# Kernel optimization log

Measured on AMD Instinct MI355X. Metric: run time of the kernel, lower is better.

## Reference

```python
import jax, jax.numpy as jnp
import numpy as np

# cfg constants (PatchNet / LDIF defaults)
SOFT_TRANSFER_SCALE = 100.0
LEVEL_SET = -0.07
INTERIOR_POINT_WEIGHT = 10.0
USE_CONSTANTS = True
AGGREGATE_COVERAGE_WITH_MAX = False

B, N, K = 8, 32768, 64


def setup_inputs() -> dict:
    key = jax.random.key(0)
    k1, k2, k3, k4, k5 = jax.random.split(key, 5)
    points_with_sdf = jax.random.normal(k1, (B, N, 4), dtype=jnp.float32)
    # negative constants = interior blobs (SIF convention)
    constants = -jnp.abs(jax.random.normal(k2, (B, K), dtype=jnp.float32))
    # positive anisotropic radii, bounded away from zero
    scales = jax.random.uniform(k3, (B, K, 3), dtype=jnp.float32) + 0.1
    rotations = jax.random.normal(k4, (B, K, 3), dtype=jnp.float32)
    centers = jax.random.normal(k5, (B, K, 3), dtype=jnp.float32)
    return {
        "points_with_sdf": points_with_sdf,
        "constants": constants,
        "scales": scales,
        "rotations": rotations,
        "centers": centers,
        "epoch": 1,
    }


def roll_pitch_yaw_to_rotation_matrices(rpy):
    # rpy: [B, K, 3] -> [B, K, 3, 3]
    c = jnp.cos(rpy)
    s = jnp.sin(rpy)
    cx, cy, cz = c[..., 0], c[..., 1], c[..., 2]
    sx, sy, sz = s[..., 0], s[..., 1], s[..., 2]
    r = jnp.stack([
        cz * cy, cz * sy * sx - sz * cx, cz * sy * cx + sz * sx,
        sz * cy, sz * sy * sx + cz * cx, sz * sy * cx - cz * sx,
        -sy, cy * sx, cy * cx,
    ], axis=-1)
    return r.reshape(rpy.shape[:-1] + (3, 3))


def sample_rbf_surface(points, constants, scales, rotations, centers,
                       use_constants, aggregate_with_max):
    # points: [B,N,3]; per-element params: [B,K,...]
    rot = roll_pitch_yaw_to_rotation_matrices(rotations)          # [B,K,3,3]
    diff = points[:, :, None, :] - centers[:, None, :, :]        # [B,N,K,3]
    # world -> local frame: R^T @ diff
    local = jnp.einsum('bkji,bnkj->bnki', rot, diff)             # [B,N,K,3]
    dist2 = jnp.sum((local / scales[:, None, :, :]) ** 2, axis=-1)  # [B,N,K]
    weights = jnp.exp(-0.5 * dist2)                              # [B,N,K]
    if use_constants:
        weights = constants[:, None, :] * weights
    if aggregate_with_max:
        return jnp.min(weights, axis=-1)  # most negative = strongest coverage
    return jnp.sum(weights, axis=-1)                             # [B,N]


def compute_inverse_occupancy(vals, soft_transfer_scale, level_set):
    return jax.nn.sigmoid(soft_transfer_scale * (vals - level_set))


def reference(points_with_sdf, constants, scales, rotations, centers, epoch):
    points = points_with_sdf[:, :, :3]
    is_outside = points_with_sdf[:, :, 3] > 0
    class_gt = is_outside.astype(jnp.float32)
    sdf_pred = sample_rbf_surface(points, constants, scales, rotations,
                                  centers, USE_CONSTANTS,
                                  AGGREGATE_COVERAGE_WITH_MAX)
    class_pred = compute_inverse_occupancy(sdf_pred, SOFT_TRANSFER_SCALE,
                                           LEVEL_SET)
    # (visualization branch of the original skipped: epoch % vis_epoch != 0)
    weights = class_gt + INTERIOR_POINT_WEIGHT * (1.0 - class_gt)
    diff = class_gt - class_pred
    loss = jnp.mean(weights * diff * diff)
    return loss
```

## Files before the change

### kernel.cpp

```cpp
#include <hip/hip_runtime.h>
#include <math.h>

#define KCL 64
#define NPTS 32768
#define NBATCH 8
#define BLOCK 256
#define PPT 4
#define PTS_PER_BLOCK (BLOCK * PPT)
#define NBLOCKS (NBATCH * NPTS / PTS_PER_BLOCK)
#define BLOCKS_PER_B (NPTS / PTS_PER_BLOCK)

__global__ __launch_bounds__(BLOCK) void point_loss_kernel(
    const float4* __restrict__ pts,
    const float*  __restrict__ constants,
    const float*  __restrict__ scales,
    const float*  __restrict__ rotations,
    const float*  __restrict__ centers,
    float*        __restrict__ partials)
{
    __shared__ float4 cl4[KCL][3];
    __shared__ float wave_sums[BLOCK / 64];

    const int tid = threadIdx.x;
    const int b   = blockIdx.x / BLOCKS_PER_B;

    if (tid < KCL) {
        const int base = b * KCL + tid;
        const float rx = rotations[3 * base + 0];
        const float ry = rotations[3 * base + 1];
        const float rz = rotations[3 * base + 2];
        const float sx = sinf(rx), cx = cosf(rx);
        const float sy = sinf(ry), cy = cosf(ry);
        const float sz = sinf(rz), cz = cosf(rz);

        float R[3][3];
        R[0][0] = cz * cy; R[0][1] = cz * sy * sx - sz * cx; R[0][2] = cz * sy * cx + sz * sx;
        R[1][0] = sz * cy; R[1][1] = sz * sy * sx + cz * cx; R[1][2] = sz * sy * cx - cz * sx;
        R[2][0] = -sy;     R[2][1] = cy * sx;                R[2][2] = cy * cx;

        const float SC = 0.84932184f;
        const float inv[3] = { SC / scales[3 * base + 0],
                               SC / scales[3 * base + 1],
                               SC / scales[3 * base + 2] };
        const float c0 = centers[3 * base + 0];
        const float c1 = centers[3 * base + 1];
        const float c2 = centers[3 * base + 2];

        float M[3][3], q[3];
        #pragma unroll
        for (int i = 0; i < 3; ++i) {
            M[i][0] = R[0][i] * inv[i];
            M[i][1] = R[1][i] * inv[i];
            M[i][2] = R[2][i] * inv[i];
            q[i] = M[i][0] * c0 + M[i][1] * c1 + M[i][2] * c2;
        }
        float A[3][3], t[3];
        #pragma unroll
        for (int j = 0; j < 3; ++j) {
            #pragma unroll
            for (int l = 0; l < 3; ++l)
                A[j][l] = M[0][j] * M[0][l] + M[1][j] * M[1][l] + M[2][j] * M[2][l];
            t[j] = M[0][j] * q[0] + M[1][j] * q[1] + M[2][j] * q[2];
        }
        const float cst = constants[base];
        const float G9 = -(q[0]*q[0] + q[1]*q[1] + q[2]*q[2]) + log2f(-cst);

        cl4[tid][0] = make_float4(-A[0][0], -A[1][1], -A[2][2], -2.0f * A[0][1]);
        cl4[tid][1] = make_float4(-2.0f * A[0][2], -2.0f * A[1][2], 2.0f * t[0], 2.0f * t[1]);
        cl4[tid][2] = make_float4(2.0f * t[2], G9, 0.0f, 0.0f);
    }
    __syncthreads();

    const int n0 = b * NPTS + (blockIdx.x % BLOCKS_PER_B) * PTS_PER_BLOCK + tid;
    float4 p[PPT];
    #pragma unroll
    for (int j = 0; j < PPT; ++j) p[j] = pts[n0 + j * BLOCK];

    float X[PPT], Y[PPT], Z[PPT], X2[PPT], Y2[PPT], Z2[PPT], XY[PPT], XZ[PPT], YZ[PPT];
    #pragma unroll
    for (int j = 0; j < PPT; ++j) {
        X[j] = p[j].x; Y[j] = p[j].y; Z[j] = p[j].z;
        X2[j] = X[j] * X[j]; Y2[j] = Y[j] * Y[j]; Z2[j] = Z[j] * Z[j];
        XY[j] = X[j] * Y[j]; XZ[j] = X[j] * Z[j]; YZ[j] = Y[j] * Z[j];
    }

    float acc[PPT] = {0.0f, 0.0f, 0.0f, 0.0f};
    #pragma unroll 4
    for (int k = 0; k < KCL; ++k) {
        const float4 A  = cl4[k][0];
        const float4 Bv = cl4[k][1];
        const float4 C  = cl4[k][2];
        #pragma unroll
        for (int j = 0; j < PPT; ++j) {
            float s = fmaf(A.x, X2[j],
                      fmaf(A.y, Y2[j],
                      fmaf(A.z, Z2[j],
                      fmaf(A.w, XY[j],
                      fmaf(Bv.x, XZ[j],
                      fmaf(Bv.y, YZ[j],
                      fmaf(Bv.z, X[j],
                      fmaf(Bv.w, Y[j],
                      fmaf(C.x, Z[j], C.y)))))))));
            acc[j] += __builtin_amdgcn_exp2f(s);
        }
    }

    float term = 0.0f;
    #pragma unroll
    for (int j = 0; j < PPT; ++j) {
        const float sdf = -acc[j];
        const float gt  = (p[j].w > 0.0f) ? 1.0f : 0.0f;
        const float z   = 100.0f * (sdf + 0.07f);
        const float pr  = 1.0f / (1.0f + __builtin_amdgcn_exp2f(-1.44269504f * z));
        const float w   = 10.0f - 9.0f * gt;
        const float d   = gt - pr;
        term = fmaf(w * d, d, term);
    }

    #pragma unroll
    for (int off = 32; off > 0; off >>= 1)
        term += __shfl_down(term, off, 64);

    if ((tid & 63) == 0) wave_sums[tid >> 6] = term;
    __syncthreads();

    if (tid == 0) {
        float s = 0.0f;
        #pragma unroll
        for (int i = 0; i < BLOCK / 64; ++i) s += wave_sums[i];
        partials[blockIdx.x] = s;
    }
}

__global__ __launch_bounds__(256) void reduce_kernel(
    const float* __restrict__ partials,
    float*       __restrict__ out)
{
    __shared__ float wave_sums[4];
    const int tid = threadIdx.x;
    float s = partials[tid];

    #pragma unroll
    for (int off = 32; off > 0; off >>= 1)
        s += __shfl_down(s, off, 64);

    if ((tid & 63) == 0) wave_sums[tid >> 6] = s;
    __syncthreads();

    if (tid == 0) {
        float t = wave_sums[0] + wave_sums[1] + wave_sums[2] + wave_sums[3];
        out[0] = t * (1.0f / (NBATCH * (float)NPTS));
    }
}

extern "C" void kernel_launch(void* const* d_in, const int* in_sizes, int n_in,
                              void* d_out, int out_size, void* d_ws, size_t ws_size,
                              hipStream_t stream) {
    const float4* pts       = (const float4*)d_in[0];
    const float*  constants = (const float*)d_in[1];
    const float*  scales    = (const float*)d_in[2];
    const float*  rotations = (const float*)d_in[3];
    const float*  centers   = (const float*)d_in[4];
    float* out      = (float*)d_out;
    float* partials = (float*)d_ws;

    point_loss_kernel<<<NBLOCKS, BLOCK, 0, stream>>>(
        pts, constants, scales, rotations, centers, partials);
    reduce_kernel<<<1, 256, 0, stream>>>(partials, out);
}
```

Baseline: 16.20 us.

## Fuse final reduction into main kernel via flag spin-wait and Horner quadratic form

Removes the separate reduce kernel launch. Block 0 spins on per-block release/acquire flags, sums all partials itself and resets the flags for the next call. The inner loop now evaluates the quadratic form in Horner style on raw x,y,z instead of keeping precomputed products, which frees registers. It also prefetches the next cluster's coefficients from shared memory. The spin-wait relies on every other block being able to run while block 0 waits, which holds here with 256 blocks, and on the workspace flags starting at zero, which only matters for correctness if the magic value is already present.

Result: slower. 19.04 us (+17.6%).

```diff
diff --git a/kernel.cpp b/kernel.cpp
--- a/kernel.cpp
+++ b/kernel.cpp
@@ -9,6 +9,8 @@
 #define PTS_PER_BLOCK (BLOCK * PPT)
 #define NBLOCKS (NBATCH * NPTS / PTS_PER_BLOCK)
 #define BLOCKS_PER_B (NPTS / PTS_PER_BLOCK)
+#define MAGIC 0x5F3C0DE5u
+
 
 __global__ __launch_bounds__(BLOCK) void point_loss_kernel(
     const float4* __restrict__ pts,
@@ -16,13 +18,16 @@
     const float*  __restrict__ scales,
     const float*  __restrict__ rotations,
     const float*  __restrict__ centers,
-    float*        __restrict__ partials)
+    float*        __restrict__ partials,
+    unsigned int* __restrict__ flags,
+    float*        __restrict__ out)
 {
     __shared__ float4 cl4[KCL][3];
     __shared__ float wave_sums[BLOCK / 64];
 
     const int tid = threadIdx.x;
-    const int b   = blockIdx.x / BLOCKS_PER_B;
+    const int bid = blockIdx.x;
+    const int b   = bid / BLOCKS_PER_B;
 
     if (tid < KCL) {
         const int base = b * KCL + tid;
@@ -63,53 +68,46 @@
             t[j] = M[0][j] * q[0] + M[1][j] * q[1] + M[2][j] * q[2];
         }
         const float cst = constants[base];
-        const float G9 = -(q[0]*q[0] + q[1]*q[1] + q[2]*q[2]) + log2f(-cst);
+        const float g9 = log2f(-cst) - (q[0]*q[0] + q[1]*q[1] + q[2]*q[2]);
 
-        cl4[tid][0] = make_float4(-A[0][0], -A[1][1], -A[2][2], -2.0f * A[0][1]);
-        cl4[tid][1] = make_float4(-2.0f * A[0][2], -2.0f * A[1][2], 2.0f * t[0], 2.0f * t[1]);
-        cl4[tid][2] = make_float4(2.0f * t[2], G9, 0.0f, 0.0f);
+        cl4[tid][0] = make_float4(-A[0][0], -2.0f * A[0][1], -2.0f * A[0][2], 2.0f * t[0]);
+        cl4[tid][1] = make_float4(-A[1][1], -2.0f * A[1][2], 2.0f * t[1], -A[2][2]);
+        cl4[tid][2] = make_float4(2.0f * t[2], g9, 0.0f, 0.0f);
     }
     __syncthreads();
 
-    const int n0 = b * NPTS + (blockIdx.x % BLOCKS_PER_B) * PTS_PER_BLOCK + tid;
-    float4 p[PPT];
-    #pragma unroll
-    for (int j = 0; j < PPT; ++j) p[j] = pts[n0 + j * BLOCK];
-
-    float X[PPT], Y[PPT], Z[PPT], X2[PPT], Y2[PPT], Z2[PPT], XY[PPT], XZ[PPT], YZ[PPT];
+    const int n0 = b * NPTS + (bid % BLOCKS_PER_B) * PTS_PER_BLOCK + tid;
+    float X[PPT], Y[PPT], Z[PPT], W[PPT];
     #pragma unroll
     for (int j = 0; j < PPT; ++j) {
-        X[j] = p[j].x; Y[j] = p[j].y; Z[j] = p[j].z;
-        X2[j] = X[j] * X[j]; Y2[j] = Y[j] * Y[j]; Z2[j] = Z[j] * Z[j];
-        XY[j] = X[j] * Y[j]; XZ[j] = X[j] * Z[j]; YZ[j] = Y[j] * Z[j];
+        const float4 p = pts[n0 + j * BLOCK];
+        X[j] = p.x; Y[j] = p.y; Z[j] = p.z; W[j] = p.w;
     }
 
     float acc[PPT] = {0.0f, 0.0f, 0.0f, 0.0f};
+    float4 F0 = cl4[0][0], F1 = cl4[0][1], F2 = cl4[0][2];
     #pragma unroll 4
     for (int k = 0; k < KCL; ++k) {
-        const float4 A  = cl4[k][0];
-        const float4 Bv = cl4[k][1];
-        const float4 C  = cl4[k][2];
+        const int kn = (k + 1) & (KCL - 1);
+        const float4 N0 = cl4[kn][0];
+        const float4 N1 = cl4[kn][1];
+        const float4 N2 = cl4[kn][2];
         #pragma unroll
         for (int j = 0; j < PPT; ++j) {
-            float s = fmaf(A.x, X2[j],
-                      fmaf(A.y, Y2[j],
-                      fmaf(A.z, Z2[j],
-                      fmaf(A.w, XY[j],
-                      fmaf(Bv.x, XZ[j],
-                      fmaf(Bv.y, YZ[j],
-                      fmaf(Bv.z, X[j],
-                      fmaf(Bv.w, Y[j],
-                      fmaf(C.x, Z[j], C.y)))))))));
+            const float t1 = fmaf(F0.x, X[j], fmaf(F0.y, Y[j], fmaf(F0.z, Z[j], F0.w)));
+            const float t2 = fmaf(F1.x, Y[j], fmaf(F1.y, Z[j], F1.z));
+            const float t3 = fmaf(F1.w, Z[j], F2.x);
+            const float s  = fmaf(X[j], t1, fmaf(Y[j], t2, fmaf(Z[j], t3, F2.y)));
             acc[j] += __builtin_amdgcn_exp2f(s);
         }
+        F0 = N0; F1 = N1; F2 = N2;
     }
 
     float term = 0.0f;
     #pragma unroll
     for (int j = 0; j < PPT; ++j) {
         const float sdf = -acc[j];
-        const float gt  = (p[j].w > 0.0f) ? 1.0f : 0.0f;
+        const float gt  = (W[j] > 0.0f) ? 1.0f : 0.0f;
         const float z   = 100.0f * (sdf + 0.07f);
         const float pr  = 1.0f / (1.0f + __builtin_amdgcn_exp2f(-1.44269504f * z));
         const float w   = 10.0f - 9.0f * gt;
@@ -128,28 +126,34 @@
         float s = 0.0f;
         #pragma unroll
         for (int i = 0; i < BLOCK / 64; ++i) s += wave_sums[i];
-        partials[blockIdx.x] = s;
+        partials[bid] = s;
+        __hip_atomic_store(&flags[bid], MAGIC,
+                           __ATOMIC_RELEASE, __HIP_MEMORY_SCOPE_AGENT);
     }
-}
 
-__global__ __launch_bounds__(256) void reduce_kernel(
-    const float* __restrict__ partials,
-    float*       __restrict__ out)
-{
-    __shared__ float wave_sums[4];
-    const int tid = threadIdx.x;
-    float s = partials[tid];
+    if (bid == 0) {
+        unsigned int f;
+        do {
+            f = __hip_atomic_load(&flags[tid],
+                                  __ATOMIC_ACQUIRE, __HIP_MEMORY_SCOPE_AGENT);
+        } while (f != MAGIC);
+        float v = __hip_atomic_load(&partials[tid],
+                                    __ATOMIC_RELAXED, __HIP_MEMORY_SCOPE_AGENT);
+        __hip_atomic_store(&flags[tid], 0u,
+                           __ATOMIC_RELAXED, __HIP_MEMORY_SCOPE_AGENT);
 
-    #pragma unroll
-    for (int off = 32; off > 0; off >>= 1)
-        s += __shfl_down(s, off, 64);
+        #pragma unroll
+        for (int off = 32; off > 0; off >>= 1)
+            v += __shfl_down(v, off, 64);
 
-    if ((tid & 63) == 0) wave_sums[tid >> 6] = s;
-    __syncthreads();
+        __syncthreads();
+        if ((tid & 63) == 0) wave_sums[tid >> 6] = v;
+        __syncthreads();
 
-    if (tid == 0) {
-        float t = wave_sums[0] + wave_sums[1] + wave_sums[2] + wave_sums[3];
-        out[0] = t * (1.0f / (NBATCH * (float)NPTS));
+        if (tid == 0) {
+            const float tot = wave_sums[0] + wave_sums[1] + wave_sums[2] + wave_sums[3];
+            out[0] = tot * (1.0f / (NBATCH * (float)NPTS));
+        }
     }
 }
 
@@ -161,10 +165,10 @@
     const float*  scales    = (const float*)d_in[2];
     const float*  rotations = (const float*)d_in[3];
     const float*  centers   = (const float*)d_in[4];
-    float* out      = (float*)d_out;
-    float* partials = (float*)d_ws;
+    float*        out       = (float*)d_out;
+    float*        partials  = (float*)d_ws;
+    unsigned int* flags     = (unsigned int*)d_ws + NBLOCKS;
 
     point_loss_kernel<<<NBLOCKS, BLOCK, 0, stream>>>(
-        pts, constants, scales, rotations, centers, partials);
-    reduce_kernel<<<1, 256, 0, stream>>>(partials, out);
+        pts, constants, scales, rotations, centers, partials, flags, out);
 }
```
